# Kernel optimization log

Hardware: AMD Instinct MI355X
Metric: run time of the kernel (lower is better)

The kernel has to match this reference:

```python
import jax, jax.numpy as jnp
import numpy as np

DEPTH = 2
DIM = 64
INNER = 256  # hard-coded inner_dim in Attention
HEADS = 1
N = 4096
B = 2
EPS = 1e-5


def layernorm(x, g, b):
    m = jnp.mean(x, axis=-1, keepdims=True)
    v = jnp.var(x, axis=-1, keepdims=True)
    return (x - m) * jax.lax.rsqrt(v + EPS) * g + b


def setup_inputs() -> dict:
    key = jax.random.key(0)
    ks = jax.random.split(key, 16)
    embed = jax.random.normal(ks[0], (B, N, DIM), dtype=jnp.float32)
    A = jax.random.randint(ks[1], (1, HEADS, N, N), 0, 2).astype(jnp.float32)
    s = 0.02
    return {
        "embed": embed,
        "A": A,
        "g1": jnp.ones((DEPTH, DIM), jnp.float32),
        "b1": jnp.zeros((DEPTH, DIM), jnp.float32),
        "Wqkv": jax.random.normal(ks[2], (DEPTH, DIM, INNER * 3), jnp.float32) * s,
        "Wout": jax.random.normal(ks[3], (DEPTH, INNER, DIM), jnp.float32) * s,
        "bout": jnp.zeros((DEPTH, DIM), jnp.float32),
        "g2": jnp.ones((DEPTH, DIM), jnp.float32),
        "b2": jnp.zeros((DEPTH, DIM), jnp.float32),
        "W1": jax.random.normal(ks[4], (DEPTH, DIM, DIM), jnp.float32) * s,
        "bb1": jnp.zeros((DEPTH, DIM), jnp.float32),
        "W2": jax.random.normal(ks[5], (DEPTH, DIM, DIM), jnp.float32) * s,
        "bb2": jnp.zeros((DEPTH, DIM), jnp.float32),
        "gf": jnp.ones((DIM,), jnp.float32),
        "bf": jnp.zeros((DIM,), jnp.float32),
    }


def _encoder(embed, A, g1, b1, Wqkv, Wout, bout, g2, b2, W1, bb1, W2, bb2, gf, bf):
    b, n, dim = embed.shape
    scale = dim ** (-0.5)
    dh = INNER // HEADS
    x = embed
    attn = None
    dots_softmax = None
    diag = jnp.arange(n)
    for l in range(DEPTH):
        xn = layernorm(x, g1[l], b1[l])
        qkv = xn @ Wqkv[l]  # [b, n, 3*INNER]
        q, k, v = jnp.split(qkv, 3, axis=-1)
        # [b, n, INNER] -> [b, h, n, dh]
        q = q.reshape(b, n, HEADS, dh).transpose(0, 2, 1, 3)
        k = k.reshape(b, n, HEADS, dh).transpose(0, 2, 1, 3)
        v = v.reshape(b, n, HEADS, dh).transpose(0, 2, 1, 3)
        dots = jnp.einsum("bhid,bhjd->bhij", q, k) * scale
        dots_softmax = jax.nn.softmax(dots[0, 0], axis=-1)
        # adjacency mask, then only [0][0] kept; diagonal filled with literal 1.0;
        # the original does a cpu/numpy roundtrip with .detach() -> stop_gradient.
        e = jnp.where(A > 0, dots, jnp.float32(-9e15))[0, 0]  # [n, n]
        e = e.at[diag, diag].set(1.0)
        e = jax.lax.stop_gradient(e)
        attn = jax.nn.softmax(e, axis=-1)  # [n, n], shared across b, h
        out = jnp.einsum("ij,bhjd->bhid", attn, v)  # broadcast attn over b,h
        out = out.transpose(0, 2, 1, 3).reshape(b, n, INNER)
        out = out @ Wout[l] + bout[l]
        x = xn + out  # residual onto the NORMED input (as in original)
        xm = layernorm(x, g2[l], b2[l])
        mlp = jax.nn.gelu(xm @ W1[l] + bb1[l], approximate=False) @ W2[l] + bb2[l]
        x = xm + mlp
    x = layernorm(x, gf, bf)
    return x, attn.reshape(1, 1, n, n), dots_softmax


def reference(embed, A, g1, b1, Wqkv, Wout, bout, g2, b2, W1, bb1, W2, bb2, gf, bf):
    return _encoder(embed, A, g1, b1, Wqkv, Wout, bout, g2, b2, W1, bb1, W2, bb2, gf, bf)
```

## Files before the change

### kernel.cpp

```cpp
#include <hip/hip_runtime.h>
#include <hip/hip_bf16.h>
#include <math.h>

typedef __attribute__((ext_vector_type(8))) short short8;
typedef __attribute__((ext_vector_type(4))) float f32x4;

#define NG 16

__device__ __forceinline__ unsigned short f2bf(float x) {
    __hip_bfloat16 b = __float2bfloat16(x);
    return *reinterpret_cast<unsigned short*>(&b);
}
__device__ __forceinline__ float bf2f(unsigned short u) {
    unsigned int t = ((unsigned int)u) << 16;
    float f;
    __builtin_memcpy(&f, &t, 4);
    return f;
}
__device__ __forceinline__ float gelu_exact(float x) {
    return 0.5f * x * (1.0f + erff(x * 0.70710678118654752f));
}

__global__ __launch_bounds__(256) void k_zero(float* __restrict__ p, long n)
{
    long i = (long)blockIdx.x * 256 + threadIdx.x;
    if (i < n) p[i] = 0.f;
}

__global__ __launch_bounds__(256) void k_layernorm(
    const float* __restrict__ x, const float* __restrict__ g,
    const float* __restrict__ b, float* __restrict__ out)
{
    int wave = threadIdx.x >> 6, lane = threadIdx.x & 63;
    long row = (long)blockIdx.x * 4 + wave;
    float v = x[row * 64 + lane];
    float s = v;
    #pragma unroll
    for (int o = 32; o; o >>= 1) s += __shfl_xor(s, o);
    float m = s * (1.0f / 64.0f);
    float d = v - m;
    float q = d * d;
    #pragma unroll
    for (int o = 32; o; o >>= 1) q += __shfl_xor(q, o);
    float rstd = rsqrtf(q * (1.0f / 64.0f) + 1e-5f);
    out[row * 64 + lane] = d * rstd * g[lane] + b[lane];
}

__global__ __launch_bounds__(256) void k_wfold(
    const float* __restrict__ Wqkv, const float* __restrict__ Wout,
    float* __restrict__ Wfold)
{
    int l = blockIdx.x >> 4;
    int idx = (blockIdx.x & 15) * 256 + threadIdx.x;
    int c = idx >> 6, d = idx & 63;
    const float* Wq = Wqkv + (long)l * 64 * 768;
    const float* Wo = Wout + (long)l * 256 * 64;
    float a = 0.f;
    for (int k = 0; k < 256; ++k)
        a += Wq[c * 768 + 512 + k] * Wo[k * 64 + d];
    Wfold[l * 4096 + idx] = a;
}

__global__ __launch_bounds__(256) void k_maskpack(
    const float* __restrict__ Aadj, unsigned long long* __restrict__ mask)
{
    int row = blockIdx.x;
    int wave = threadIdx.x >> 6, lane = threadIdx.x & 63;
    for (int w = wave; w < 64; w += 4) {
        float a = Aadj[(long)row * 4096 + w * 64 + lane];
        unsigned long long m = __ballot(a > 0.f);
        if (lane == 0) mask[(long)row * 64 + w] = m;
    }
}

__global__ __launch_bounds__(256) void k_qk(
    const float* __restrict__ xn, const float* __restrict__ W,
    unsigned short* __restrict__ q, unsigned short* __restrict__ kmat)
{
    __shared__ float As[64][65];
    __shared__ float Ws[64][65];
    int tid = threadIdx.x;
    int m0 = blockIdx.x * 64, n0 = blockIdx.y * 64;
    #pragma unroll
    for (int it = 0; it < 16; ++it) {
        int idx = tid + it * 256;
        int r = idx >> 6, c = idx & 63;
        As[r][c] = xn[(long)(m0 + r) * 64 + c];
        Ws[r][c] = W[(long)r * 768 + n0 + c];
    }
    __syncthreads();
    int tx = tid & 15, ty = tid >> 4;
    float acc[4][4] = {};
    #pragma unroll
    for (int k = 0; k < 64; ++k) {
        float a[4], w[4];
        #pragma unroll
        for (int i = 0; i < 4; ++i) a[i] = As[ty * 4 + i][k];
        #pragma unroll
        for (int j = 0; j < 4; ++j) w[j] = Ws[k][tx * 4 + j];
        #pragma unroll
        for (int i = 0; i < 4; ++i)
            #pragma unroll
            for (int j = 0; j < 4; ++j) acc[i][j] += a[i] * w[j];
    }
    #pragma unroll
    for (int i = 0; i < 4; ++i) {
        long row = m0 + ty * 4 + i;
        #pragma unroll
        for (int j = 0; j < 4; ++j) {
            int col = n0 + tx * 4 + j;
            if (col < 256) q[row * 256 + col] = f2bf(acc[i][j]);
            else           kmat[row * 256 + (col - 256)] = f2bf(acc[i][j]);
        }
    }
}

__global__ __launch_bounds__(256) void k_xnw_t(
    const float* __restrict__ xn, const float* __restrict__ Wfold,
    unsigned short* __restrict__ vWT)
{
    __shared__ float As[64][65];
    __shared__ float Ws[64][65];
    int tid = threadIdx.x;
    int n0 = blockIdx.x * 64, b = blockIdx.y;
    #pragma unroll
    for (int it = 0; it < 16; ++it) {
        int idx = tid + it * 256;
        int r = idx >> 6, c = idx & 63;
        As[r][c] = xn[((long)b * 4096 + n0 + r) * 64 + c];
        Ws[r][c] = Wfold[r * 64 + c];
    }
    __syncthreads();
    int tx = tid & 15, ty = tid >> 4;
    float acc[4][4] = {};
    #pragma unroll
    for (int k = 0; k < 64; ++k) {
        float a[4], w[4];
        #pragma unroll
        for (int i = 0; i < 4; ++i) a[i] = As[ty * 4 + i][k];
        #pragma unroll
        for (int j = 0; j < 4; ++j) w[j] = Ws[k][tx * 4 + j];
        #pragma unroll
        for (int i = 0; i < 4; ++i)
            #pragma unroll
            for (int j = 0; j < 4; ++j) acc[i][j] += a[i] * w[j];
    }
    #pragma unroll
    for (int i = 0; i < 4; ++i)
        #pragma unroll
        for (int j = 0; j < 4; ++j)
            vWT[((long)b * 64 + tx * 4 + j) * 4096 + n0 + ty * 4 + i] = f2bf(acc[i][j]);
}

__global__ __launch_bounds__(256) void k_flash(
    const unsigned short* __restrict__ q, const unsigned short* __restrict__ kmat,
    const unsigned short* __restrict__ vwt,
    const unsigned long long* __restrict__ mask, const float* __restrict__ Aadj,
    unsigned short* __restrict__ part,
    float* __restrict__ stats)
{
    __shared__ __align__(16) unsigned short Qs[128 * 64];
    __shared__ __align__(16) unsigned short Ks[128 * 64];
    __shared__ __align__(16) unsigned short Ps[128 * 128];
    int tid = threadIdx.x;
    int lane = tid & 63, wq = tid >> 6;
    int fr = lane & 15, quad = lane >> 4;
    int m0 = blockIdx.x * 128;
    int g  = blockIdx.y;

    f32x4 accO[2][8];
    #pragma unroll
    for (int i = 0; i < 2; ++i)
        #pragma unroll
        for (int j = 0; j < 8; ++j) accO[i][j] = (f32x4){0.f, 0.f, 0.f, 0.f};
    float m_run[2] = {-1e30f, -1e30f};
    float s_run[2] = {0.f, 0.f};

    for (int jt = 0; jt < 2; ++jt) {
        int jb = g * 256 + jt * 128;
        f32x4 accS[8][2];
        #pragma unroll
        for (int i = 0; i < 8; ++i)
            #pragma unroll
            for (int n = 0; n < 2; ++n) accS[i][n] = (f32x4){0.f, 0.f, 0.f, 0.f};
        for (int k0 = 0; k0 < 256; k0 += 64) {
            #pragma unroll
            for (int it = 0; it < 4; ++it) {
                int idx = tid + it * 256;
                int r = idx >> 3, c8 = (idx & 7) * 8;
                *(short8*)&Qs[idx * 8] = *(const short8*)(q    + (long)(m0 + r) * 256 + k0 + c8);
                *(short8*)&Ks[idx * 8] = *(const short8*)(kmat + (long)(jb + r) * 256 + k0 + c8);
            }
            __syncthreads();
            #pragma unroll
            for (int ks = 0; ks < 2; ++ks) {
                short8 ka[8], qb[2];
                #pragma unroll
                for (int i = 0; i < 8; ++i)
                    ka[i] = *(const short8*)&Ks[(i * 16 + fr) * 64 + ks * 32 + quad * 8];
                #pragma unroll
                for (int n = 0; n < 2; ++n)
                    qb[n] = *(const short8*)&Qs[(wq * 32 + n * 16 + fr) * 64 + ks * 32 + quad * 8];
                #pragma unroll
                for (int i = 0; i < 8; ++i)
// ... 62 lines not shown
                for (int r = 0; r < 4; ++r) accO[ii][nn][r] *= av[r];
        }
        #pragma unroll
        for (int it = 0; it < 4; ++it) {
            int idx = tid + it * 256;
            int r = idx >> 3, c8 = (idx & 7) * 8;
            *(short8*)&Qs[idx * 8] = *(const short8*)(vwt + (long)r * 4096 + jb + c8);
            *(short8*)&Ks[idx * 8] = *(const short8*)(vwt + (long)r * 4096 + jb + 64 + c8);
        }
        __syncthreads();
        #pragma unroll
        for (int ks4 = 0; ks4 < 4; ++ks4) {
            const unsigned short* buf = (ks4 < 2) ? Qs : Ks;
            int ksl = ks4 & 1;
            short8 pa[2], vb[8];
            #pragma unroll
            for (int ii = 0; ii < 2; ++ii) {
                int u = ((wq * 32 + ii * 16 + fr) * 128 + ks4 * 32 + quad * 8) ^ ((fr & 7) << 3);
                pa[ii] = *(const short8*)&Ps[u];
            }
            #pragma unroll
            for (int nn = 0; nn < 8; ++nn)
                vb[nn] = *(const short8*)&buf[(nn * 16 + fr) * 64 + ksl * 32 + quad * 8];
            #pragma unroll
            for (int ii = 0; ii < 2; ++ii)
                #pragma unroll
                for (int nn = 0; nn < 8; ++nn)
                    accO[ii][nn] = __builtin_amdgcn_mfma_f32_16x16x32_bf16(
                        pa[ii], vb[nn], accO[ii][nn], 0, 0, 0);
        }
        __syncthreads();
    }
    #pragma unroll
    for (int ii = 0; ii < 2; ++ii) {
        #pragma unroll
        for (int nn = 0; nn < 8; ++nn) {
            int ch = nn * 16 + fr;
            long rowb = m0 + wq * 32 + ii * 16 + quad * 4;
            #pragma unroll
            for (int r = 0; r < 4; ++r)
                part[((long)g * 4096 + rowb + r) * 128 + ch] = f2bf(accO[ii][nn][r]);
        }
    }
    if (quad == 0) {
        #pragma unroll
        for (int n = 0; n < 2; ++n) {
            int qrow = m0 + wq * 32 + n * 16 + fr;
            stats[((long)g * 4096 + qrow) * 2]     = m_run[n];
            stats[((long)g * 4096 + qrow) * 2 + 1] = s_run[n];
        }
    }
}

__global__ __launch_bounds__(256) void k_mfma_nt(
    const unsigned short* __restrict__ A, const unsigned short* __restrict__ B,
    float* __restrict__ C, int N, int K, float scale)
{
    __shared__ __align__(16) unsigned short As[128 * 64];
    __shared__ __align__(16) unsigned short Bs[128 * 64];
    int tid = threadIdx.x;
    int lane = tid & 63, wave = tid >> 6;
    long m0 = (long)blockIdx.x * 128, n0 = (long)blockIdx.y * 128;
    const unsigned short* Ag = A + m0 * K;
    const unsigned short* Bg = B + n0 * K;
    int wm = (wave & 1) * 64, wn = (wave >> 1) * 64;
    int fr = lane & 15, quad = lane >> 4;

    f32x4 acc[4][4];
    #pragma unroll
    for (int i = 0; i < 4; ++i)
        #pragma unroll
        for (int j = 0; j < 4; ++j) acc[i][j] = (f32x4){0.f, 0.f, 0.f, 0.f};

    for (int k0 = 0; k0 < K; k0 += 64) {
        #pragma unroll
        for (int it = 0; it < 4; ++it) {
            int c = tid + it * 256;
            int r = c >> 3, col = (c & 7) * 8;
            *(short8*)&As[c * 8] = *(const short8*)(Ag + (long)r * K + k0 + col);
            *(short8*)&Bs[c * 8] = *(const short8*)(Bg + (long)r * K + k0 + col);
        }
        __syncthreads();
        #pragma unroll
        for (int ks = 0; ks < 2; ++ks) {
            short8 af[4], bfr[4];
            #pragma unroll
            for (int i = 0; i < 4; ++i) {
                af[i]  = *(const short8*)&As[(wm + i * 16 + fr) * 64 + ks * 32 + quad * 8];
                bfr[i] = *(const short8*)&Bs[(wn + i * 16 + fr) * 64 + ks * 32 + quad * 8];
            }
            #pragma unroll
            for (int i = 0; i < 4; ++i)
                #pragma unroll
                for (int j = 0; j < 4; ++j)
                    acc[i][j] = __builtin_amdgcn_mfma_f32_16x16x32_bf16(
                        af[i], bfr[j], acc[i][j], 0, 0, 0);
        }
        __syncthreads();
    }
    #pragma unroll
    for (int i = 0; i < 4; ++i) {
        #pragma unroll
        for (int j = 0; j < 4; ++j) {
            long col = n0 + wn + j * 16 + fr;
            long rowb = m0 + wm + i * 16 + quad * 4;
            #pragma unroll
            for (int r = 0; r < 4; ++r)
                C[(rowb + r) * N + col] = acc[i][j][r] * scale;
        }
    }
}

__global__ __launch_bounds__(256) void k_mfma_splitk(
    const float* __restrict__ A, const unsigned short* __restrict__ B,
    float* __restrict__ C)
{
    __shared__ __align__(16) unsigned short As[128 * 64];
    __shared__ __align__(16) unsigned short Bs[128 * 64];
    const int K = 4096, N = 128;
    int tid = threadIdx.x;
    int lane = tid & 63, wave = tid >> 6;
    long m0 = (long)blockIdx.x * 128;
    int k0base = blockIdx.y * 512;
    const float* Ag = A + m0 * K;
    int wm = (wave & 1) * 64, wn = (wave >> 1) * 64;
    int fr = lane & 15, quad = lane >> 4;

    f32x4 acc[4][4];
    #pragma unroll
    for (int i = 0; i < 4; ++i)
        #pragma unroll
        for (int j = 0; j < 4; ++j) acc[i][j] = (f32x4){0.f, 0.f, 0.f, 0.f};

    for (int k0 = k0base; k0 < k0base + 512; k0 += 64) {
        #pragma unroll
        for (int it = 0; it < 4; ++it) {
            int c = tid + it * 256;
            int r = c >> 3, col = (c & 7) * 8;
            float4 f0 = *(const float4*)(Ag + (long)r * K + k0 + col);
            float4 f1 = *(const float4*)(Ag + (long)r * K + k0 + col + 4);
            short8 s;
            s[0] = (short)f2bf(f0.x); s[1] = (short)f2bf(f0.y);
            s[2] = (short)f2bf(f0.z); s[3] = (short)f2bf(f0.w);
            s[4] = (short)f2bf(f1.x); s[5] = (short)f2bf(f1.y);
            s[6] = (short)f2bf(f1.z); s[7] = (short)f2bf(f1.w);
            *(short8*)&As[c * 8] = s;
            *(short8*)&Bs[c * 8] = *(const short8*)(B + (long)r * K + k0 + col);
        }
        __syncthreads();
        #pragma unroll
        for (int ks = 0; ks < 2; ++ks) {
            short8 af[4], bfr[4];
            #pragma unroll
            for (int i = 0; i < 4; ++i) {
                af[i]  = *(const short8*)&As[(wm + i * 16 + fr) * 64 + ks * 32 + quad * 8];
                bfr[i] = *(const short8*)&Bs[(wn + i * 16 + fr) * 64 + ks * 32 + quad * 8];
            }
            #pragma unroll
            for (int i = 0; i < 4; ++i)
                #pragma unroll
                for (int j = 0; j < 4; ++j)
                    acc[i][j] = __builtin_amdgcn_mfma_f32_16x16x32_bf16(
                        af[i], bfr[j], acc[i][j], 0, 0, 0);
        }
        __syncthreads();
    }
    #pragma unroll
    for (int i = 0; i < 4; ++i) {
        #pragma unroll
        for (int j = 0; j < 4; ++j) {
            long col = wn + j * 16 + fr;
            long rowb = m0 + wm + i * 16 + quad * 4;
            #pragma unroll
            for (int r = 0; r < 4; ++r)
                atomicAdd(&C[(rowb + r) * N + col], acc[i][j][r]);
        }
    }
}

__device__ __forceinline__ float block_max(float v, float* red, int lane, int wave) {
    #pragma unroll
    for (int o = 32; o; o >>= 1) v = fmaxf(v, __shfl_xor(v, o));
    if (lane == 0) red[wave] = v;
    __syncthreads();
    v = fmaxf(fmaxf(red[0], red[1]), fmaxf(red[2], red[3]));
    __syncthreads();
    return v;
}
__device__ __forceinline__ float block_sum(float v, float* red, int lane, int wave) {
    #pragma unroll
    for (int o = 32; o; o >>= 1) v += __shfl_xor(v, o);
    if (lane == 0) red[wave] = v;
    __syncthreads();
    v = red[0] + red[1] + red[2] + red[3];
    __syncthreads();
    return v;
}

__global__ __launch_bounds__(256) void k_softmax_attn(
    float* __restrict__ dots, const float* __restrict__ Aadj,
    const unsigned long long* __restrict__ mask,
    float* __restrict__ attn_out, int write_ds)
{
    __shared__ float red[4];
    __shared__ unsigned long long msk[64];
    int row = blockIdx.x, tid = threadIdx.x;
    int lane = tid & 63, wave = tid >> 6;
    float* drow = dots + (long)row * 4096;
    if (mask) {
        if (tid < 64) msk[tid] = mask[(long)row * 64 + tid];
        __syncthreads();
    }
    float d[16], mv[16];
    float mmax = -1e30f, umax = -1e30f;
    #pragma unroll
    for (int i = 0; i < 16; ++i) {
        int j = tid + i * 256;
        float dv = drow[j];
        d[i] = dv;
        bool keep = mask ? ((msk[j >> 6] >> (j & 63)) & 1ull)
                         : (Aadj[(long)row * 4096 + j] > 0.f);
        float m = keep ? dv : -1e30f;
        if (j == row) m = 1.0f;
        mv[i] = m;
        mmax = fmaxf(mmax, m);
        umax = fmaxf(umax, dv);
    }
    float M1 = block_max(mmax, red, lane, wave);
    float s1 = 0.f;
    #pragma unroll
    for (int i = 0; i < 16; ++i) { float e = expf(mv[i] - M1); mv[i] = e; s1 += e; }
    s1 = block_sum(s1, red, lane, wave);
    float inv1 = 1.0f / s1;
    #pragma unroll
    for (int i = 0; i < 16; ++i)
        attn_out[(long)row * 4096 + tid + i * 256] = mv[i] * inv1;

    if (write_ds) {
        float M2 = block_max(umax, red, lane, wave);
        float s2 = 0.f;
        #pragma unroll
        for (int i = 0; i < 16; ++i) { float e = expf(d[i] - M2); d[i] = e; s2 += e; }
        s2 = block_sum(s2, red, lane, wave);
        float inv2 = 1.0f / s2;
        #pragma unroll
        for (int i = 0; i < 16; ++i)
            drow[tid + i * 256] = d[i] * inv2;
    }
}

__global__ __launch_bounds__(256) void k_avres_ln(
    const float* __restrict__ xn, const float* __restrict__ avcat,
    const float* __restrict__ bout, const float* __restrict__ g,
    const float* __restrict__ b, float* __restrict__ out)
{
    int wave = threadIdx.x >> 6, lane = threadIdx.x & 63;
    long row = (long)blockIdx.x * 4 + wave;
    int bb = (int)(row >> 12), n = (int)(row & 4095);
    float v = xn[row * 64 + lane] + avcat[(long)n * 128 + bb * 64 + lane] + bout[lane];
    float s = v;
    #pragma unroll
    for (int o = 32; o; o >>= 1) s += __shfl_xor(s, o);
    float m = s * (1.0f / 64.0f);
    float d = v - m;
    float q = d * d;
    #pragma unroll
    for (int o = 32; o; o >>= 1) q += __shfl_xor(q, o);
    float rstd = rsqrtf(q * (1.0f / 64.0f) + 1e-5f);
    out[row * 64 + lane] = d * rstd * g[lane] + b[lane];
}

__global__ __launch_bounds__(256) void k_avres_ln_c(
    const float* __restrict__ xn, const unsigned short* __restrict__ part,
    const float* __restrict__ stats, const float* __restrict__ bout,
    const float* __restrict__ g, const float* __restrict__ b,
    float* __restrict__ out)
{
    int wave = threadIdx.x >> 6, lane = threadIdx.x & 63;
    long row = (long)blockIdx.x * 4 + wave;
    int bb = (int)(row >> 12), n = (int)(row & 4095);
    float sm[NG], ss[NG];
    float ms = -1e30f;
    #pragma unroll
    for (int gg = 0; gg < NG; ++gg) {
        sm[gg] = stats[((long)gg * 4096 + n) * 2];
        ss[gg] = stats[((long)gg * 4096 + n) * 2 + 1];
        ms = fmaxf(ms, sm[gg]);
    }
    float acc = 0.f, stot = 0.f;
    #pragma unroll
    for (int gg = 0; gg < NG; ++gg) {
        float w = __expf(sm[gg] - ms);
        stot += w * ss[gg];
        acc  += w * bf2f(part[((long)gg * 4096 + n) * 128 + bb * 64 + lane]);
    }
    float v = xn[row * 64 + lane] + acc / stot + bout[lane];
    float s = v;
    #pragma unroll
    for (int o = 32; o; o >>= 1) s += __shfl_xor(s, o);
    float m = s * (1.0f / 64.0f);
    float d = v - m;
    float qv = d * d;
    #pragma unroll
    for (int o = 32; o; o >>= 1) qv += __shfl_xor(qv, o);
    float rstd = rsqrtf(qv * (1.0f / 64.0f) + 1e-5f);
    out[row * 64 + lane] = d * rstd * g[lane] + b[lane];
}

__global__ __launch_bounds__(256) void k_mlp(
    const float* __restrict__ xm,
    const float* __restrict__ W1, const float* __restrict__ bb1,
    const float* __restrict__ W2, const float* __restrict__ bb2,
    const float* __restrict__ g, const float* __restrict__ b,
    float* __restrict__ out)
{
    __shared__ float As[64][65];
    __shared__ float W1s[64][65];
    __shared__ float W2s[64][65];
    int tid = threadIdx.x;
    int m0 = blockIdx.x * 64;
    #pragma unroll
    for (int it = 0; it < 16; ++it) {
        int idx = tid + it * 256;
        int r = idx >> 6, c = idx & 63;
        As[r][c]  = xm[(long)(m0 + r) * 64 + c];
        W1s[r][c] = W1[(long)r * 64 + c];
        W2s[r][c] = W2[(long)r * 64 + c];
    }
    __syncthreads();
    int tx = tid & 15, ty = tid >> 4;
    float acc[4][4] = {};
    #pragma unroll
    for (int k = 0; k < 64; ++k) {
        float a[4], w[4];
        #pragma unroll
        for (int i = 0; i < 4; ++i) a[i] = As[ty * 4 + i][k];
        #pragma unroll
        for (int j = 0; j < 4; ++j) w[j] = W1s[k][tx * 4 + j];
        #pragma unroll
        for (int i = 0; i < 4; ++i)
            #pragma unroll
            for (int j = 0; j < 4; ++j) acc[i][j] += a[i] * w[j];
    }
    __syncthreads();
    #pragma unroll
    for (int i = 0; i < 4; ++i)
        #pragma unroll
        for (int j = 0; j < 4; ++j)
            W1s[ty * 4 + i][tx * 4 + j] = gelu_exact(acc[i][j] + bb1[tx * 4 + j]);
    __syncthreads();
    float acc2[4][4] = {};
    #pragma unroll
    for (int k = 0; k < 64; ++k) {
        float a[4], w[4];
        #pragma unroll
        for (int i = 0; i < 4; ++i) a[i] = W1s[ty * 4 + i][k];
        #pragma unroll
        for (int j = 0; j < 4; ++j) w[j] = W2s[k][tx * 4 + j];
        #pragma unroll
        for (int i = 0; i < 4; ++i)
            #pragma unroll
            for (int j = 0; j < 4; ++j) acc2[i][j] += a[i] * w[j];
    }
    #pragma unroll
    for (int i = 0; i < 4; ++i) {
        float v[4];
        float s = 0.f;
        #pragma unroll
        for (int j = 0; j < 4; ++j) {
            v[j] = acc2[i][j] + bb2[tx * 4 + j] + As[ty * 4 + i][tx * 4 + j];
            s += v[j];
        }
        #pragma unroll
        for (int o = 1; o < 16; o <<= 1) s += __shfl_xor(s, o);
        float m = s * (1.0f / 64.0f);
        float q = 0.f;
        #pragma unroll
        for (int j = 0; j < 4; ++j) { float d = v[j] - m; q += d * d; }
        #pragma unroll
        for (int o = 1; o < 16; o <<= 1) q += __shfl_xor(q, o);
        float rstd = rsqrtf(q * (1.0f / 64.0f) + 1e-5f);
        long row = m0 + ty * 4 + i;
        #pragma unroll
        for (int j = 0; j < 4; ++j) {
            int col = tx * 4 + j;
            out[row * 64 + col] = (v[j] - m) * rstd * g[col] + b[col];
        }
    }
}

extern "C" void kernel_launch(void* const* d_in, const int* in_sizes, int n_in,
                              void* d_out, int out_size, void* d_ws, size_t ws_size,
                              hipStream_t stream)
{
    const float* embed = (const float*)d_in[0];
    const float* Aadj  = (const float*)d_in[1];
    const float* g1    = (const float*)d_in[2];
    const float* b1    = (const float*)d_in[3];
    const float* Wqkv  = (const float*)d_in[4];
    const float* Wout  = (const float*)d_in[5];
    const float* bout  = (const float*)d_in[6];
    const float* g2    = (const float*)d_in[7];
    const float* b2    = (const float*)d_in[8];
    const float* W1    = (const float*)d_in[9];
    const float* bb1   = (const float*)d_in[10];
    const float* W2    = (const float*)d_in[11];
    const float* bb2   = (const float*)d_in[12];
    const float* gf    = (const float*)d_in[13];
    const float* bff   = (const float*)d_in[14];

    float* ox    = (float*)d_out;
    float* attnb = ox + 524288;
    float* dsb   = attnb + 16777216;

    if (ws_size < (10ull << 20)) {
        k_zero<<<133120, 256, 0, stream>>>(ox, 34078720l);
        return;
    }

    char* ws = (char*)d_ws;
    float*          xn    = (float*)(ws + (2l << 20));
    unsigned short* q     = (unsigned short*)(ws + (6l << 20));
    unsigned short* kmat  = (unsigned short*)(ws + (7l << 20));
    unsigned short* vwt   = (unsigned short*)(ws + (8l << 20));
    float*          Wfold = (float*)(ws + (9l << 20));
    unsigned long long* mask = (ws_size >= (12ull << 20))
        ? (unsigned long long*)(ws + (10l << 20)) : nullptr;

    unsigned short* part   = (unsigned short*)attnb;
    float*          fstats = attnb + 4194304;

    if (mask) k_maskpack<<<4096, 256, 0, stream>>>(Aadj, mask);
    k_wfold<<<32, 256, 0, stream>>>(Wqkv, Wout, Wfold);

    k_layernorm<<<2048, 256, 0, stream>>>(embed, g1, b1, xn);
    k_qk<<<dim3(64, 8), 256, 0, stream>>>(xn, Wqkv, q, kmat);
    k_xnw_t<<<dim3(64, 2), 256, 0, stream>>>(xn, Wfold, vwt);
    k_flash<<<dim3(32, NG), 256, 0, stream>>>(q, kmat, vwt, mask, Aadj, part, fstats);
    k_avres_ln_c<<<2048, 256, 0, stream>>>(xn, part, fstats, bout, g2, b2, xn);
    k_mlp<<<128, 256, 0, stream>>>(xn, W1, bb1, W2, bb2,
                                   g1 + 64, b1 + 64, xn);

    k_qk<<<dim3(64, 8), 256, 0, stream>>>(xn, Wqkv + 64 * 768, q, kmat);
    k_xnw_t<<<dim3(64, 2), 256, 0, stream>>>(xn, Wfold + 4096, vwt);
    k_mfma_nt<<<dim3(32, 32), 256, 0, stream>>>(q, kmat, dsb, 4096, 256, 0.125f);
    k_softmax_attn<<<4096, 256, 0, stream>>>(dsb, Aadj, mask, attnb, 1);
    k_zero<<<2048, 256, 0, stream>>>(ox, 524288l);
    k_mfma_splitk<<<dim3(32, 8), 256, 0, stream>>>(attnb, vwt, ox);
    k_avres_ln<<<2048, 256, 0, stream>>>(xn, ox, bout + 64, g2 + 64, b2 + 64, xn);
    k_mlp<<<128, 256, 0, stream>>>(xn, W1 + 4096, bb1 + 64, W2 + 4096, bb2 + 64,
                                   gf, bff, ox);
}
```

Before: 463.9 us.

## Fuse prologue kernels, merge QK/V projections, and compute final-layer attention in two passes

Mask packing, weight folding, the first layernorm and output zeroing are merged into one prologue launch. The Q/K and folded-V projections are merged into one grid, and the attention-output residual plus layernorm is folded into the MLP kernel. For the last layer, the separate dots GEMM and softmax pass over a materialized dots buffer are replaced by two kernels. The first computes per-group online softmax stats for both the masked and the plain softmax, and the second recomputes QK^T and writes attn and dots_softmax directly. This removes several launches and a full N×N read-back, but QK^T is now computed twice in the last layer.

```diff
diff --git a/kernel.cpp b/kernel.cpp
--- a/kernel.cpp
+++ b/kernel.cpp
@@ -27,129 +27,128 @@
     if (i < n) p[i] = 0.f;
 }
 
-__global__ __launch_bounds__(256) void k_layernorm(
-    const float* __restrict__ x, const float* __restrict__ g,
-    const float* __restrict__ b, float* __restrict__ out)
-{
-    int wave = threadIdx.x >> 6, lane = threadIdx.x & 63;
-    long row = (long)blockIdx.x * 4 + wave;
-    float v = x[row * 64 + lane];
-    float s = v;
-    #pragma unroll
-    for (int o = 32; o; o >>= 1) s += __shfl_xor(s, o);
-    float m = s * (1.0f / 64.0f);
-    float d = v - m;
-    float q = d * d;
-    #pragma unroll
-    for (int o = 32; o; o >>= 1) q += __shfl_xor(q, o);
-    float rstd = rsqrtf(q * (1.0f / 64.0f) + 1e-5f);
-    out[row * 64 + lane] = d * rstd * g[lane] + b[lane];
-}
-
-__global__ __launch_bounds__(256) void k_wfold(
+__global__ __launch_bounds__(256) void k_prologue(
+    const float* __restrict__ Aadj, unsigned long long* __restrict__ mask,
     const float* __restrict__ Wqkv, const float* __restrict__ Wout,
-    float* __restrict__ Wfold)
-{
-    int l = blockIdx.x >> 4;
-    int idx = (blockIdx.x & 15) * 256 + threadIdx.x;
-    int c = idx >> 6, d = idx & 63;
-    const float* Wq = Wqkv + (long)l * 64 * 768;
-    const float* Wo = Wout + (long)l * 256 * 64;
-    float a = 0.f;
-    for (int k = 0; k < 256; ++k)
-        a += Wq[c * 768 + 512 + k] * Wo[k * 64 + d];
-    Wfold[l * 4096 + idx] = a;
-}
-
-__global__ __launch_bounds__(256) void k_maskpack(
-    const float* __restrict__ Aadj, unsigned long long* __restrict__ mask)
-{
-    int row = blockIdx.x;
-    int wave = threadIdx.x >> 6, lane = threadIdx.x & 63;
-    for (int w = wave; w < 64; w += 4) {
-        float a = Aadj[(long)row * 4096 + w * 64 + lane];
-        unsigned long long m = __ballot(a > 0.f);
-        if (lane == 0) mask[(long)row * 64 + w] = m;
-    }
-}
-
-__global__ __launch_bounds__(256) void k_qk(
+    float* __restrict__ Wfold,
+    const float* __restrict__ embed, const float* __restrict__ g1,
+    const float* __restrict__ b1, float* __restrict__ xn,
+    float* __restrict__ zbuf)
+{
+    int bx = blockIdx.x, tid = threadIdx.x;
+    if (bx < 4096) {
+        if (!mask) return;
+        int row = bx;
+        int wave = tid >> 6, lane = tid & 63;
+        for (int w = wave; w < 64; w += 4) {
+            float a = Aadj[(long)row * 4096 + w * 64 + lane];
+            unsigned long long m = __ballot(a > 0.f);
+            if (lane == 0) mask[(long)row * 64 + w] = m;
+        }
+    } else if (bx < 4128) {
+        int bid = bx - 4096;
+        int l = bid >> 4;
+        int idx = (bid & 15) * 256 + tid;
+        int c = idx >> 6, d = idx & 63;
+        const float* Wq = Wqkv + (long)l * 64 * 768;
+        const float* Wo = Wout + (long)l * 256 * 64;
+        float a = 0.f;
+        for (int k = 0; k < 256; ++k)
+            a += Wq[c * 768 + 512 + k] * Wo[k * 64 + d];
+        Wfold[l * 4096 + idx] = a;
+    } else if (bx < 6176) {
+        int wave = tid >> 6, lane = tid & 63;
+        long row = (long)(bx - 4128) * 4 + wave;
+        float v = embed[row * 64 + lane];
+        float s = v;
+        #pragma unroll
+        for (int o = 32; o; o >>= 1) s += __shfl_xor(s, o);
+        float m = s * (1.0f / 64.0f);
+        float d = v - m;
+        float q = d * d;
+        #pragma unroll
+        for (int o = 32; o; o >>= 1) q += __shfl_xor(q, o);
+        float rstd = rsqrtf(q * (1.0f / 64.0f) + 1e-5f);
+        xn[row * 64 + lane] = d * rstd * g1[lane] + b1[lane];
+    } else {
+        long i = (long)(bx - 6176) * 256 + tid;
+        if (i < 524288) zbuf[i] = 0.f;
+    }
+}
+
+__global__ __launch_bounds__(256) void k_qkx(
     const float* __restrict__ xn, const float* __restrict__ W,
-    unsigned short* __restrict__ q, unsigned short* __restrict__ kmat)
+    const float* __restrict__ Wfold,
+    unsigned short* __restrict__ q, unsigned short* __restrict__ kmat,
+    unsigned short* __restrict__ vWT)
 {
     __shared__ float As[64][65];
     __shared__ float Ws[64][65];
     int tid = threadIdx.x;
-    int m0 = blockIdx.x * 64, n0 = blockIdx.y * 64;
-    #pragma unroll
-    for (int it = 0; it < 16; ++it) {
-        int idx = tid + it * 256;
-        int r = idx >> 6, c = idx & 63;
-        As[r][c] = xn[(long)(m0 + r) * 64 + c];
-        Ws[r][c] = W[(long)r * 768 + n0 + c];
-    }
-    __syncthreads();
+    int by = blockIdx.y;
     int tx = tid & 15, ty = tid >> 4;
-    float acc[4][4] = {};
-    #pragma unroll
-    for (int k = 0; k < 64; ++k) {
-        float a[4], w[4];
-        #pragma unroll
-        for (int i = 0; i < 4; ++i) a[i] = As[ty * 4 + i][k];
-        #pragma unroll
-        for (int j = 0; j < 4; ++j) w[j] = Ws[k][tx * 4 + j];
+    if (by < 8) {
+        int m0 = blockIdx.x * 64, n0 = by * 64;
+        #pragma unroll
+        for (int it = 0; it < 16; ++it) {
+            int idx = tid + it * 256;
+            int r = idx >> 6, c = idx & 63;
+            As[r][c] = xn[(long)(m0 + r) * 64 + c];
+            Ws[r][c] = W[(long)r * 768 + n0 + c];
+        }
+        __syncthreads();
+        float acc[4][4] = {};
+        #pragma unroll
+        for (int k = 0; k < 64; ++k) {
+            float a[4], w[4];
+            #pragma unroll
+            for (int i = 0; i < 4; ++i) a[i] = As[ty * 4 + i][k];
+            #pragma unroll
+            for (int j = 0; j < 4; ++j) w[j] = Ws[k][tx * 4 + j];
+            #pragma unroll
+            for (int i = 0; i < 4; ++i)
+                #pragma unroll
+                for (int j = 0; j < 4; ++j) acc[i][j] += a[i] * w[j];
+        }
+        #pragma unroll
+        for (int i = 0; i < 4; ++i) {
+            long row = m0 + ty * 4 + i;
+            #pragma unroll
+            for (int j = 0; j < 4; ++j) {
+                int col = n0 + tx * 4 + j;
+                if (col < 256) q[row * 256 + col] = f2bf(acc[i][j]);
+                else           kmat[row * 256 + (col - 256)] = f2bf(acc[i][j]);
+            }
+        }
+    } else {
+        int n0 = blockIdx.x * 64, b = by - 8;
+        #pragma unroll
+        for (int it = 0; it < 16; ++it) {
+            int idx = tid + it * 256;
+            int r = idx >> 6, c = idx & 63;
+            As[r][c] = xn[((long)b * 4096 + n0 + r) * 64 + c];
+            Ws[r][c] = Wfold[r * 64 + c];
+        }
+        __syncthreads();
+        float acc[4][4] = {};
+        #pragma unroll
+        for (int k = 0; k < 64; ++k) {
+            float a[4], w[4];
+            #pragma unroll
+            for (int i = 0; i < 4; ++i) a[i] = As[ty * 4 + i][k];
+            #pragma unroll
+            for (int j = 0; j < 4; ++j) w[j] = Ws[k][tx * 4 + j];
+            #pragma unroll
+            for (int i = 0; i < 4; ++i)
+                #pragma unroll
+                for (int j = 0; j < 4; ++j) acc[i][j] += a[i] * w[j];
+        }
         #pragma unroll
         for (int i = 0; i < 4; ++i)
             #pragma unroll
-            for (int j = 0; j < 4; ++j) acc[i][j] += a[i] * w[j];
-    }
-    #pragma unroll
-    for (int i = 0; i < 4; ++i) {
-        long row = m0 + ty * 4 + i;
-        #pragma unroll
-        for (int j = 0; j < 4; ++j) {
-            int col = n0 + tx * 4 + j;
-            if (col < 256) q[row * 256 + col] = f2bf(acc[i][j]);
-            else           kmat[row * 256 + (col - 256)] = f2bf(acc[i][j]);
-        }
-    }
-}
-
-__global__ __launch_bounds__(256) void k_xnw_t(
-    const float* __restrict__ xn, const float* __restrict__ Wfold,
-    unsigned short* __restrict__ vWT)
-{
-    __shared__ float As[64][65];
-    __shared__ float Ws[64][65];
-    int tid = threadIdx.x;
-    int n0 = blockIdx.x * 64, b = blockIdx.y;
-    #pragma unroll
-    for (int it = 0; it < 16; ++it) {
-        int idx = tid + it * 256;
-        int r = idx >> 6, c = idx & 63;
-        As[r][c] = xn[((long)b * 4096 + n0 + r) * 64 + c];
-        Ws[r][c] = Wfold[r * 64 + c];
-    }
-    __syncthreads();
-    int tx = tid & 15, ty = tid >> 4;
-    float acc[4][4] = {};
-    #pragma unroll
-    for (int k = 0; k < 64; ++k) {
-        float a[4], w[4];
-        #pragma unroll
-        for (int i = 0; i < 4; ++i) a[i] = As[ty * 4 + i][k];
-        #pragma unroll
-        for (int j = 0; j < 4; ++j) w[j] = Ws[k][tx * 4 + j];
-        #pragma unroll
-        for (int i = 0; i < 4; ++i)
-            #pragma unroll
-            for (int j = 0; j < 4; ++j) acc[i][j] += a[i] * w[j];
-    }
-    #pragma unroll
-    for (int i = 0; i < 4; ++i)
-        #pragma unroll
-        for (int j = 0; j < 4; ++j)
-            vWT[((long)b * 64 + tx * 4 + j) * 4096 + n0 + ty * 4 + i] = f2bf(acc[i][j]);
+            for (int j = 0; j < 4; ++j)
+                vWT[((long)b * 64 + tx * 4 + j) * 4096 + n0 + ty * 4 + i] = f2bf(acc[i][j]);
+    }
 }
 
 __global__ __launch_bounds__(256) void k_flash(
@@ -318,61 +317,212 @@
     }
 }
 
-__global__ __launch_bounds__(256) void k_mfma_nt(
-    const unsigned short* __restrict__ A, const unsigned short* __restrict__ B,
-    float* __restrict__ C, int N, int K, float scale)
-{
-    __shared__ __align__(16) unsigned short As[128 * 64];
-    __shared__ __align__(16) unsigned short Bs[128 * 64];
+__global__ __launch_bounds__(256) void k_stats(
+    const unsigned short* __restrict__ q, const unsigned short* __restrict__ kmat,
+    const unsigned long long* __restrict__ mask, const float* __restrict__ Aadj,
+    float* __restrict__ stats2)
+{
+    __shared__ __align__(16) unsigned short Qs[128 * 64];
+    __shared__ __align__(16) unsigned short Ks[128 * 64];
     int tid = threadIdx.x;
-    int lane = tid & 63, wave = tid >> 6;
-    long m0 = (long)blockIdx.x * 128, n0 = (long)blockIdx.y * 128;
-    const unsigned short* Ag = A + m0 * K;
-    const unsigned short* Bg = B + n0 * K;
-    int wm = (wave & 1) * 64, wn = (wave >> 1) * 64;
+    int lane = tid & 63, wq = tid >> 6;
     int fr = lane & 15, quad = lane >> 4;
-
-    f32x4 acc[4][4];
-    #pragma unroll
-    for (int i = 0; i < 4; ++i)
-        #pragma unroll
-        for (int j = 0; j < 4; ++j) acc[i][j] = (f32x4){0.f, 0.f, 0.f, 0.f};
-
-    for (int k0 = 0; k0 < K; k0 += 64) {
-        #pragma unroll
-        for (int it = 0; it < 4; ++it) {
-            int c = tid + it * 256;
-            int r = c >> 3, col = (c & 7) * 8;
-            *(short8*)&As[c * 8] = *(const short8*)(Ag + (long)r * K + k0 + col);
-            *(short8*)&Bs[c * 8] = *(const short8*)(Bg + (long)r * K + k0 + col);
-        }
-        __syncthreads();
-        #pragma unroll
-        for (int ks = 0; ks < 2; ++ks) {
-            short8 af[4], bfr[4];
-            #pragma unroll
-            for (int i = 0; i < 4; ++i) {
-                af[i]  = *(const short8*)&As[(wm + i * 16 + fr) * 64 + ks * 32 + quad * 8];
-                bfr[i] = *(const short8*)&Bs[(wn + i * 16 + fr) * 64 + ks * 32 + quad * 8];
-            }
-            #pragma unroll
-            for (int i = 0; i < 4; ++i)
-                #pragma unroll
-                for (int j = 0; j < 4; ++j)
-                    acc[i][j] = __builtin_amdgcn_mfma_f32_16x16x32_bf16(
-                        af[i], bfr[j], acc[i][j], 0, 0, 0);
-        }
-        __syncthreads();
-    }
-    #pragma unroll
-    for (int i = 0; i < 4; ++i) {
-        #pragma unroll
-        for (int j = 0; j < 4; ++j) {
-            long col = n0 + wn + j * 16 + fr;
-            long rowb = m0 + wm + i * 16 + quad * 4;
-            #pragma unroll
-            for (int r = 0; r < 4; ++r)
-                C[(rowb + r) * N + col] = acc[i][j][r] * scale;
+    int m0 = blockIdx.x * 128;
+    int g  = blockIdx.y;
+    float m1[2] = {-1e30f, -1e30f}, s1[2] = {0.f, 0.f};
+    float m2[2] = {-1e30f, -1e30f}, s2[2] = {0.f, 0.f};
+
+    for (int jt = 0; jt < 2; ++jt) {
+        int jb = g * 256 + jt * 128;
+        f32x4 accS[8][2];
+        #pragma unroll
+        for (int i = 0; i < 8; ++i)
+            #pragma unroll
+            for (int n = 0; n < 2; ++n) accS[i][n] = (f32x4){0.f, 0.f, 0.f, 0.f};
+        for (int k0 = 0; k0 < 256; k0 += 64) {
+            #pragma unroll
+            for (int it = 0; it < 4; ++it) {
+                int idx = tid + it * 256;
+                int r = idx >> 3, c8 = (idx & 7) * 8;
+                *(short8*)&Qs[idx * 8] = *(const short8*)(q    + (long)(m0 + r) * 256 + k0 + c8);
+                *(short8*)&Ks[idx * 8] = *(const short8*)(kmat + (long)(jb + r) * 256 + k0 + c8);
+            }
+            __syncthreads();
+            #pragma unroll
+            for (int ks = 0; ks < 2; ++ks) {
+                short8 ka[8], qb[2];
+                #pragma unroll
+                for (int i = 0; i < 8; ++i)
+                    ka[i] = *(const short8*)&Ks[(i * 16 + fr) * 64 + ks * 32 + quad * 8];
+                #pragma unroll
+                for (int n = 0; n < 2; ++n)
+                    qb[n] = *(const short8*)&Qs[(wq * 32 + n * 16 + fr) * 64 + ks * 32 + quad * 8];
+                #pragma unroll
+                for (int i = 0; i < 8; ++i)
+                    #pragma unroll
+                    for (int n = 0; n < 2; ++n)
+                        accS[i][n] = __builtin_amdgcn_mfma_f32_16x16x32_bf16(
+                            ka[i], qb[n], accS[i][n], 0, 0, 0);
+            }
+            __syncthreads();
+        }
+        #pragma unroll
+        for (int n = 0; n < 2; ++n) {
+            int qrow = m0 + wq * 32 + n * 16 + fr;
+            unsigned long long mw0 = 0, mw1 = 0;
+            if (mask) {
+                mw0 = mask[(long)qrow * 64 + (jb >> 6)];
+                mw1 = mask[(long)qrow * 64 + (jb >> 6) + 1];
+            }
+            float tm1 = -1e30f, tm2 = -1e30f;
+            #pragma unroll
+            for (int i = 0; i < 8; ++i) {
+                #pragma unroll
+                for (int r = 0; r < 4; ++r) {
+                    int jl = i * 16 + quad * 4 + r;
+                    float v = accS[i][n][r] * 0.125f;
+                    accS[i][n][r] = v;
+                    tm2 = fmaxf(tm2, v);
+                    bool keep = mask ? (((jl < 64 ? (mw0 >> jl) : (mw1 >> (jl - 64))) & 1ull) != 0)
+                                     : (Aadj[(long)qrow * 4096 + jb + jl] > 0.f);
+                    float mv = keep ? v : -1e30f;
+                    if (jb + jl == qrow) mv = 1.0f;
+                    tm1 = fmaxf(tm1, mv);
+                }
+            }
+            tm1 = fmaxf(tm1, __shfl_xor(tm1, 16));
+            tm1 = fmaxf(tm1, __shfl_xor(tm1, 32));
+            tm2 = fmaxf(tm2, __shfl_xor(tm2, 16));
+            tm2 = fmaxf(tm2, __shfl_xor(tm2, 32));
+            float mn1 = fmaxf(fmaxf(m1[n], tm1), -1e20f);
+            float mn2 = fmaxf(fmaxf(m2[n], tm2), -1e20f);
+            float a1 = __expf(m1[n] - mn1), a2 = __expf(m2[n] - mn2);
+            float ts1 = 0.f, ts2 = 0.f;
+            #pragma unroll
+            for (int i = 0; i < 8; ++i) {
+                #pragma unroll
+                for (int r = 0; r < 4; ++r) {
+                    int jl = i * 16 + quad * 4 + r;
+                    float v = accS[i][n][r];
+                    ts2 += __expf(v - mn2);
+                    bool keep = mask ? (((jl < 64 ? (mw0 >> jl) : (mw1 >> (jl - 64))) & 1ull) != 0)
+                                     : (Aadj[(long)qrow * 4096 + jb + jl] > 0.f);
+                    float mv = keep ? v : -1e30f;
+                    if (jb + jl == qrow) mv = 1.0f;
+                    ts1 += __expf(mv - mn1);
+                }
+            }
+            ts1 += __shfl_xor(ts1, 16); ts1 += __shfl_xor(ts1, 32);
+            ts2 += __shfl_xor(ts2, 16); ts2 += __shfl_xor(ts2, 32);
+            s1[n] = s1[n] * a1 + ts1; m1[n] = mn1;
+            s2[n] = s2[n] * a2 + ts2; m2[n] = mn2;
+        }
+    }
+    if (quad == 0) {
+        #pragma unroll
+        for (int n = 0; n < 2; ++n) {
+            int qrow = m0 + wq * 32 + n * 16 + fr;
+            *(float4*)&stats2[(long)qrow * 64 + g * 4] =
+                make_float4(m1[n], s1[n], m2[n], s2[n]);
+        }
+    }
+}
+
+__global__ __launch_bounds__(256) void k_attn_ds(
+    const unsigned short* __restrict__ q, const unsigned short* __restrict__ kmat,
+    const unsigned long long* __restrict__ mask, const float* __restrict__ Aadj,
+    const float* __restrict__ stats2,
+    float* __restrict__ attn, float* __restrict__ ds)
+{
+    __shared__ __align__(16) unsigned short Qs[128 * 64];
+    __shared__ __align__(16) unsigned short Ks[128 * 64];
+    int tid = threadIdx.x;
+    int lane = tid & 63, wq = tid >> 6;
+    int fr = lane & 15, quad = lane >> 4;
+    int m0 = blockIdx.x * 128;
+    int g  = blockIdx.y;
+
+    float M1[2], S1i[2], M2[2], S2i[2];
+    #pragma unroll
+    for (int n = 0; n < 2; ++n) {
+        int qrow = m0 + wq * 32 + n * 16 + fr;
+        float mm1 = -1e30f, mm2 = -1e30f;
+        for (int gg = 0; gg < NG; ++gg) {
+            float4 s4 = *(const float4*)&stats2[(long)qrow * 64 + gg * 4];
+            mm1 = fmaxf(mm1, s4.x);
+            mm2 = fmaxf(mm2, s4.z);
+        }
+        float ss1 = 0.f, ss2 = 0.f;
+        for (int gg = 0; gg < NG; ++gg) {
+            float4 s4 = *(const float4*)&stats2[(long)qrow * 64 + gg * 4];
+            ss1 += s4.y * __expf(s4.x - mm1);
+            ss2 += s4.w * __expf(s4.z - mm2);
+        }
+        M1[n] = mm1; S1i[n] = 1.0f / ss1;
+        M2[n] = mm2; S2i[n] = 1.0f / ss2;
+    }
+
+    for (int jt = 0; jt < 2; ++jt) {
+        int jb = g * 256 + jt * 128;
+        f32x4 accS[8][2];
+        #pragma unroll
+        for (int i = 0; i < 8; ++i)
+            #pragma unroll
+            for (int n = 0; n < 2; ++n) accS[i][n] = (f32x4){0.f, 0.f, 0.f, 0.f};
+        for (int k0 = 0; k0 < 256; k0 += 64) {
+            #pragma unroll
+            for (int it = 0; it < 4; ++it) {
+                int idx = tid + it * 256;
+                int r = idx >> 3, c8 = (idx & 7) * 8;
+                *(short8*)&Qs[idx * 8] = *(const short8*)(q    + (long)(m0 + r) * 256 + k0 + c8);
+                *(short8*)&Ks[idx * 8] = *(const short8*)(kmat + (long)(jb + r) * 256 + k0 + c8);
+            }
+            __syncthreads();
+            #pragma unroll
+            for (int ks = 0; ks < 2; ++ks) {
+                short8 ka[8], qb[2];
+                #pragma unroll
+                for (int i = 0; i < 8; ++i)
+                    ka[i] = *(const short8*)&Ks[(i * 16 + fr) * 64 + ks * 32 + quad * 8];
+                #pragma unroll
+                for (int n = 0; n < 2; ++n)
+                    qb[n] = *(const short8*)&Qs[(wq * 32 + n * 16 + fr) * 64 + ks * 32 + quad * 8];
+                #pragma unroll
+                for (int i = 0; i < 8; ++i)
+                    #pragma unroll
+                    for (int n = 0; n < 2; ++n)
+                        accS[i][n] = __builtin_amdgcn_mfma_f32_16x16x32_bf16(
+                            ka[i], qb[n], accS[i][n], 0, 0, 0);
+            }
+            __syncthreads();
+        }
+        #pragma unroll
+        for (int n = 0; n < 2; ++n) {
+            int qrow = m0 + wq * 32 + n * 16 + fr;
+            unsigned long long mw0 = 0, mw1 = 0;
+            if (mask) {
+                mw0 = mask[(long)qrow * 64 + (jb >> 6)];
+                mw1 = mask[(long)qrow * 64 + (jb >> 6) + 1];
+            }
+            #pragma unroll
+            for (int i = 0; i < 8; ++i) {
+                float4 du, da;
+                float* dup = &du.x; float* dap = &da.x;
+                #pragma unroll
+                for (int r = 0; r < 4; ++r) {
+                    int jl = i * 16 + quad * 4 + r;
+                    float v = accS[i][n][r] * 0.125f;
+                    dup[r] = __expf(v - M2[n]) * S2i[n];
+                    bool keep = mask ? (((jl < 64 ? (mw0 >> jl) : (mw1 >> (jl - 64))) & 1ull) != 0)
+                                     : (Aadj[(long)qrow * 4096 + jb + jl] > 0.f);
+                    float mv = keep ? v : -1e30f;
+                    if (jb + jl == qrow) mv = 1.0f;
+                    dap[r] = __expf(mv - M1[n]) * S1i[n];
+                }
+                long off = (long)qrow * 4096 + jb + i * 16 + quad * 4;
+                *(float4*)&ds[off]   = du;
+                *(float4*)&attn[off] = da;
+            }
         }
     }
 }
@@ -444,157 +594,83 @@
     }
 }
 
-__device__ __forceinline__ float block_max(float v, float* red, int lane, int wave) {
-    #pragma unroll
-    for (int o = 32; o; o >>= 1) v = fmaxf(v, __shfl_xor(v, o));
-    if (lane == 0) red[wave] = v;
-    __syncthreads();
-    v = fmaxf(fmaxf(red[0], red[1]), fmaxf(red[2], red[3]));
-    __syncthreads();
-    return v;
-}
-__device__ __forceinline__ float block_sum(float v, float* red, int lane, int wave) {
-    #pragma unroll
-    for (int o = 32; o; o >>= 1) v += __shfl_xor(v, o);
-    if (lane == 0) red[wave] = v;
-    __syncthreads();
-    v = red[0] + red[1] + red[2] + red[3];
-    __syncthreads();
-    return v;
-}
-
-__global__ __launch_bounds__(256) void k_softmax_attn(
-    float* __restrict__ dots, const float* __restrict__ Aadj,
-    const unsigned long long* __restrict__ mask,
-    float* __restrict__ attn_out, int write_ds)
-{
-    __shared__ float red[4];
-    __shared__ unsigned long long msk[64];
-    int row = blockIdx.x, tid = threadIdx.x;
-    int lane = tid & 63, wave = tid >> 6;
-    float* drow = dots + (long)row * 4096;
-    if (mask) {
-        if (tid < 64) msk[tid] = mask[(long)row * 64 + tid];
-        __syncthreads();
-    }
-    float d[16], mv[16];
-    float mmax = -1e30f, umax = -1e30f;
-    #pragma unroll
-    for (int i = 0; i < 16; ++i) {
-        int j = tid + i * 256;
-        float dv = drow[j];
-        d[i] = dv;
-        bool keep = mask ? ((msk[j >> 6] >> (j & 63)) & 1ull)
-                         : (Aadj[(long)row * 4096 + j] > 0.f);
-        float m = keep ? dv : -1e30f;
-        if (j == row) m = 1.0f;
-        mv[i] = m;
-        mmax = fmaxf(mmax, m);
-        umax = fmaxf(umax, dv);
-    }
-    float M1 = block_max(mmax, red, lane, wave);
-    float s1 = 0.f;
-    #pragma unroll
-    for (int i = 0; i < 16; ++i) { float e = expf(mv[i] - M1); mv[i] = e; s1 += e; }
-    s1 = block_sum(s1, red, lane, wave);
-    float inv1 = 1.0f / s1;
-    #pragma unroll
-    for (int i = 0; i < 16; ++i)
-        attn_out[(long)row * 4096 + tid + i * 256] = mv[i] * inv1;
-
-    if (write_ds) {
-        float M2 = block_max(umax, red, lane, wave);
-        float s2 = 0.f;
-        #pragma unroll
-        for (int i = 0; i < 16; ++i) { float e = expf(d[i] - M2); d[i] = e; s2 += e; }
-        s2 = block_sum(s2, red, lane, wave);
-        float inv2 = 1.0f / s2;
-        #pragma unroll
-        for (int i = 0; i < 16; ++i)
-            drow[tid + i * 256] = d[i] * inv2;
-    }
-}
-
-__global__ __launch_bounds__(256) void k_avres_ln(
-    const float* __restrict__ xn, const float* __restrict__ avcat,
-    const float* __restrict__ bout, const float* __restrict__ g,
-    const float* __restrict__ b, float* __restrict__ out)
-{
-    int wave = threadIdx.x >> 6, lane = threadIdx.x & 63;
-    long row = (long)blockIdx.x * 4 + wave;
-    int bb = (int)(row >> 12), n = (int)(row & 4095);
-    float v = xn[row * 64 + lane] + avcat[(long)n * 128 + bb * 64 + lane] + bout[lane];
-    float s = v;
-    #pragma unroll
-    for (int o = 32; o; o >>= 1) s += __shfl_xor(s, o);
-    float m = s * (1.0f / 64.0f);
-    float d = v - m;
-    float q = d * d;
-    #pragma unroll
-    for (int o = 32; o; o >>= 1) q += __shfl_xor(q, o);
-    float rstd = rsqrtf(q * (1.0f / 64.0f) + 1e-5f);
-    out[row * 64 + lane] = d * rstd * g[lane] + b[lane];
-}
-
-__global__ __launch_bounds__(256) void k_avres_ln_c(
-    const float* __restrict__ xn, const unsigned short* __restrict__ part,
-    const float* __restrict__ stats, const float* __restrict__ bout,
-    const float* __restrict__ g, const float* __restrict__ b,
-    float* __restrict__ out)
-{
-    int wave = threadIdx.x >> 6, lane = threadIdx.x & 63;
-    long row = (long)blockIdx.x * 4 + wave;
-    int bb = (int)(row >> 12), n = (int)(row & 4095);
-    float sm[NG], ss[NG];
-    float ms = -1e30f;
-    #pragma unroll
-    for (int gg = 0; gg < NG; ++gg) {
-        sm[gg] = stats[((long)gg * 4096 + n) * 2];
-        ss[gg] = stats[((long)gg * 4096 + n) * 2 + 1];
-        ms = fmaxf(ms, sm[gg]);
-    }
-    float acc = 0.f, stot = 0.f;
-    #pragma unroll
-    for (int gg = 0; gg < NG; ++gg) {
-        float w = __expf(sm[gg] - ms);
-        stot += w * ss[gg];
-        acc  += w * bf2f(part[((long)gg * 4096 + n) * 128 + bb * 64 + lane]);
-    }
-    float v = xn[row * 64 + lane] + acc / stot + bout[lane];
-    float s = v;
-    #pragma unroll
-    for (int o = 32; o; o >>= 1) s += __shfl_xor(s, o);
-    float m = s * (1.0f / 64.0f);
-    float d = v - m;
-    float qv = d * d;
-    #pragma unroll
-    for (int o = 32; o; o >>= 1) qv += __shfl_xor(qv, o);
-    float rstd = rsqrtf(qv * (1.0f / 64.0f) + 1e-5f);
-    out[row * 64 + lane] = d * rstd * g[lane] + b[lane];
-}
-
 __global__ __launch_bounds__(256) void k_mlp(
-    const float* __restrict__ xm,
+    int mode, const float* __restrict__ xn,
+    const unsigned short* __restrict__ part, const float* __restrict__ fstats,
+    const float* __restrict__ avcat, const float* __restrict__ boutv,
+    const float* __restrict__ gin, const float* __restrict__ bin,
     const float* __restrict__ W1, const float* __restrict__ bb1,
     const float* __restrict__ W2, const float* __restrict__ bb2,
-    const float* __restrict__ g, const float* __restrict__ b,
+    const float* __restrict__ gout, const float* __restrict__ bln,
     float* __restrict__ out)
 {
     __shared__ float As[64][65];
     __shared__ float W1s[64][65];
     __shared__ float W2s[64][65];
+    __shared__ float wg[64][NG];
     int tid = threadIdx.x;
     int m0 = blockIdx.x * 64;
+    if (mode == 0 && tid < 64) {
+        int n = (m0 + tid) & 4095;
+        float mg[NG], sg[NG];
+        float mx = -1e30f;
+        #pragma unroll
+        for (int g = 0; g < NG; ++g) {
+            mg[g] = fstats[((long)g * 4096 + n) * 2];
+            sg[g] = fstats[((long)g * 4096 + n) * 2 + 1];
+            mx = fmaxf(mx, mg[g]);
+        }
+        float stot = 0.f;
+        float w[NG];
+        #pragma unroll
+        for (int g = 0; g < NG; ++g) { w[g] = __expf(mg[g] - mx); stot += w[g] * sg[g]; }
+        float inv = 1.0f / stot;
+        #pragma unroll
+        for (int g = 0; g < NG; ++g) wg[tid][g] = w[g] * inv;
+    }
+    __syncthreads();
     #pragma unroll
     for (int it = 0; it < 16; ++it) {
         int idx = tid + it * 256;
         int r = idx >> 6, c = idx & 63;
-        As[r][c]  = xm[(long)(m0 + r) * 64 + c];
+        long row = m0 + r;
+        int n = (int)(row & 4095), bb = (int)(row >> 12);
+        float v = xn[row * 64 + c] + boutv[c];
+        if (mode == 0) {
+            #pragma unroll
+            for (int g = 0; g < NG; ++g)
+                v += wg[r][g] * bf2f(part[((long)g * 4096 + n) * 128 + bb * 64 + c]);
+        } else {
+            v += avcat[(long)n * 128 + bb * 64 + c];
+        }
+        As[r][c]  = v;
         W1s[r][c] = W1[(long)r * 64 + c];
         W2s[r][c] = W2[(long)r * 64 + c];
     }
     __syncthreads();
     int tx = tid & 15, ty = tid >> 4;
+    #pragma unroll
+    for (int i = 0; i < 4; ++i) {
+        float vv[4];
+        float s = 0.f;
+        #pragma unroll
+        for (int j = 0; j < 4; ++j) { vv[j] = As[ty * 4 + i][tx * 4 + j]; s += vv[j]; }
+        #pragma unroll
+        for (int o = 1; o < 16; o <<= 1) s += __shfl_xor(s, o);
+        float m = s * (1.0f / 64.0f);
+        float qv = 0.f;
+        #pragma unroll
+        for (int j = 0; j < 4; ++j) { float d = vv[j] - m; qv += d * d; }
+        #pragma unroll
+        for (int o = 1; o < 16; o <<= 1) qv += __shfl_xor(qv, o);
+        float rstd = rsqrtf(qv * (1.0f / 64.0f) + 1e-5f);
+        #pragma unroll
+        for (int j = 0; j < 4; ++j) {
+            int col = tx * 4 + j;
+            As[ty * 4 + i][col] = (vv[j] - m) * rstd * gin[col] + bin[col];
+        }
+    }
+    __syncthreads();
     float acc[4][4] = {};
     #pragma unroll
     for (int k = 0; k < 64; ++k) {
@@ -640,17 +716,17 @@
         #pragma unroll
         for (int o = 1; o < 16; o <<= 1) s += __shfl_xor(s, o);
         float m = s * (1.0f / 64.0f);
-        float q = 0.f;
-        #pragma unroll
-        for (int j = 0; j < 4; ++j) { float d = v[j] - m; q += d * d; }
-        #pragma unroll
-        for (int o = 1; o < 16; o <<= 1) q += __shfl_xor(q, o);
-        float rstd = rsqrtf(q * (1.0f / 64.0f) + 1e-5f);
+        float qv = 0.f;
+        #pragma unroll
+        for (int j = 0; j < 4; ++j) { float d = v[j] - m; qv += d * d; }
+        #pragma unroll
+        for (int o = 1; o < 16; o <<= 1) qv += __shfl_xor(qv, o);
+        float rstd = rsqrtf(qv * (1.0f / 64.0f) + 1e-5f);
         long row = m0 + ty * 4 + i;
         #pragma unroll
         for (int j = 0; j < 4; ++j) {
             int col = tx * 4 + j;
-            out[row * 64 + col] = (v[j] - m) * rstd * g[col] + b[col];
+            out[row * 64 + col] = (v[j] - m) * rstd * gout[col] + bln[col];
         }
     }
 }
@@ -685,35 +761,33 @@
     }
 
     char* ws = (char*)d_ws;
-    float*          xn    = (float*)(ws + (2l << 20));
-    unsigned short* q     = (unsigned short*)(ws + (6l << 20));
-    unsigned short* kmat  = (unsigned short*)(ws + (7l << 20));
-    unsigned short* vwt   = (unsigned short*)(ws + (8l << 20));
-    float*          Wfold = (float*)(ws + (9l << 20));
+    float*          avcat  = (float*)(ws + (0l << 20));
+    float*          xn     = (float*)(ws + (2l << 20));
+    float*          stats2 = (float*)(ws + (4l << 20));
+    unsigned short* q      = (unsigned short*)(ws + (6l << 20));
+    unsigned short* kmat   = (unsigned short*)(ws + (7l << 20));
+    unsigned short* vwt    = (unsigned short*)(ws + (8l << 20));
+    float*          Wfold  = (float*)(ws + (9l << 20));
     unsigned long long* mask = (ws_size >= (12ull << 20))
         ? (unsigned long long*)(ws + (10l << 20)) : nullptr;
 
     unsigned short* part   = (unsigned short*)attnb;
     float*          fstats = attnb + 4194304;
 
-    if (mask) k_maskpack<<<4096, 256, 0, stream>>>(Aadj, mask);
-    k_wfold<<<32, 256, 0, stream>>>(Wqkv, Wout, Wfold);
-
-    k_layernorm<<<2048, 256, 0, stream>>>(embed, g1, b1, xn);
-    k_qk<<<dim3(64, 8), 256, 0, stream>>>(xn, Wqkv, q, kmat);
-    k_xnw_t<<<dim3(64, 2), 256, 0, stream>>>(xn, Wfold, vwt);
+    k_prologue<<<8224, 256, 0, stream>>>(Aadj, mask, Wqkv, Wout, Wfold,
+                                         embed, g1, b1, xn, avcat);
+
+    k_qkx<<<dim3(64, 10), 256, 0, stream>>>(xn, Wqkv, Wfold, q, kmat, vwt);
     k_flash<<<dim3(32, NG), 256, 0, stream>>>(q, kmat, vwt, mask, Aadj, part, fstats);
-    k_avres_ln_c<<<2048, 256, 0, stream>>>(xn, part, fstats, bout, g2, b2, xn);
-    k_mlp<<<128, 256, 0, stream>>>(xn, W1, bb1, W2, bb2,
+    k_mlp<<<128, 256, 0, stream>>>(0, xn, part, fstats, nullptr, bout,
+                                   g2, b2, W1, bb1, W2, bb2,
                                    g1 + 64, b1 + 64, xn);
 
-    k_qk<<<dim3(64, 8), 256, 0, stream>>>(xn, Wqkv + 64 * 768, q, kmat);
-    k_xnw_t<<<dim3(64, 2), 256, 0, stream>>>(xn, Wfold + 4096, vwt);
-    k_mfma_nt<<<dim3(32, 32), 256, 0, stream>>>(q, kmat, dsb, 4096, 256, 0.125f);
-    k_softmax_attn<<<4096, 256, 0, stream>>>(dsb, Aadj, mask, attnb, 1);
-    k_zero<<<2048, 256, 0, stream>>>(ox, 524288l);
-    k_mfma_splitk<<<dim3(32, 8), 256, 0, stream>>>(attnb, vwt, ox);
-    k_avres_ln<<<2048, 256, 0, stream>>>(xn, ox, bout + 64, g2 + 64, b2 + 64, xn);
-    k_mlp<<<128, 256, 0, stream>>>(xn, W1 + 4096, bb1 + 64, W2 + 4096, bb2 + 64,
+    k_qkx<<<dim3(64, 10), 256, 0, stream>>>(xn, Wqkv + 64 * 768, Wfold + 4096, q, kmat, vwt);
+    k_stats<<<dim3(32, NG), 256, 0, stream>>>(q, kmat, mask, Aadj, stats2);
+    k_attn_ds<<<dim3(32, NG), 256, 0, stream>>>(q, kmat, mask, Aadj, stats2, attnb, dsb);
+    k_mfma_splitk<<<dim3(32, 8), 256, 0, stream>>>(attnb, vwt, avcat);
+    k_mlp<<<128, 256, 0, stream>>>(1, xn, nullptr, nullptr, avcat, bout + 64,
+                                   g2 + 64, b2 + 64, W1 + 4096, bb1 + 64, W2 + 4096, bb2 + 64,
                                    gf, bff, ox);
 }
```

After: 513.1 us. 10.6% more time.
